# Optimization experiments

Measured on AMD Instinct MI355X. Metric: run time of the kernel, lower is better.

The kernel has to match this reference:

```python
import jax, jax.numpy as jnp
import numpy as np

B, S_ENC, S_DEC, D_ENC, D_DEC, UNITS = 8, 256, 128, 512, 512, 512


def setup_inputs() -> dict:
    key = jax.random.key(0)
    ks = jax.random.split(key, 5)
    enc_scale = 1.0 / np.sqrt(D_ENC)
    dec_scale = 1.0 / np.sqrt(D_DEC)
    u_scale = 1.0 / np.sqrt(UNITS)
    return {
        "encodings": jax.random.normal(ks[0], (B, S_ENC, D_ENC), dtype=jnp.float32),
        "decodings": jax.random.normal(ks[1], (B, S_DEC, D_DEC), dtype=jnp.float32),
        "W_enc": jax.random.normal(ks[2], (D_ENC, UNITS), dtype=jnp.float32) * enc_scale,
        "W_dec": jax.random.normal(ks[3], (D_DEC, UNITS), dtype=jnp.float32) * dec_scale,
        "W_score": jax.random.normal(ks[4], (UNITS, 1), dtype=jnp.float32) * u_scale,
        "bias_enc": jnp.zeros((UNITS,), dtype=jnp.float32),
        "bias_dec": jnp.zeros((UNITS,), dtype=jnp.float32),
        "bias_score": jnp.zeros((1,), dtype=jnp.float32),
    }


def reference(encodings, decodings, W_enc, W_dec, W_score, bias_enc, bias_dec, bias_score):
    # activation='linear' -> identity after the bias add
    d_enc = jnp.einsum("bed,du->beu", encodings, W_enc) + bias_enc  # [B, S_enc, U]
    d_dec = jnp.einsum("bqd,du->bqu", decodings, W_dec) + bias_dec  # [B, S_dec, U]
    # Bahdanau additive scores: tanh(dec_proj + enc_proj) broadcast to [B, S_dec, S_enc, U]
    tanh_add = jnp.tanh(d_dec[:, :, None, :] + d_enc[:, None, :, :])
    scores = jnp.einsum("bqeu,u->bqe", tanh_add, W_score[:, 0]) + bias_score[0]
    weights = jax.nn.softmax(scores, axis=-1)  # softmax over encoder positions
    # weighted sum of raw encodings -> [B, S_dec, D_enc]
    contexts = jnp.einsum("bqe,bed->bqd", weights, encodings)
    return contexts
```

## Files before the change

### kernel.cpp

```cpp
#include <hip/hip_runtime.h>
#include <hip/hip_fp16.h>

typedef __attribute__((ext_vector_type(8))) _Float16 f16x8;
typedef __attribute__((ext_vector_type(4))) float f32x4;
typedef __attribute__((ext_vector_type(2))) __fp16 fp16x2;

__device__ inline unsigned int pack_f16(float x, float y) {
    union { fp16x2 h; unsigned int u; } c;
    c.h = __builtin_amdgcn_cvt_pkrtz(x, y);
    return c.u;
}
__device__ inline float2 unpack_f16(unsigned int u) {
    union { unsigned int u32; __half2 h2; } c; c.u32 = u;
    return __half22float2(c.h2);
}

__global__ __launch_bounds__(256) void prep_w(
    const float* __restrict__ Wenc, const float* __restrict__ Wdec,
    const float* __restrict__ enc,  const float* __restrict__ dec,
    unsigned short* __restrict__ WeT, unsigned short* __restrict__ WdT,
    unsigned short* __restrict__ enc16, unsigned short* __restrict__ dec16)
{
    __shared__ float L[64][65];
    const int bid = blockIdx.x;
    const int t = threadIdx.x;
    if (bid >= 128) {
        const float* src; unsigned int* dst;
        if (bid < 192) { int blk = bid - 128; src = enc + (size_t)blk * 16384;
                         dst = (unsigned int*)enc16 + (size_t)blk * 8192; }
        else           { int blk = bid - 192; src = dec + (size_t)blk * 16384;
                         dst = (unsigned int*)dec16 + (size_t)blk * 8192; }
#pragma unroll 4
        for (int i = 0; i < 16; ++i) {
            int off = (i << 10) + (t << 2);
            float4 v = *(const float4*)(src + off);
            *(uint2*)(dst + (off >> 1)) =
                make_uint2(pack_f16(v.x, v.y), pack_f16(v.z, v.w));
        }
        return;
    }
    const float* W = (bid < 64) ? Wenc : Wdec;
    unsigned short* T = (bid < 64) ? WeT : WdT;
    const int tb = bid & 63;
    const int d0 = (tb >> 3) << 6, u0v = (tb & 7) << 6;
    {
        const int c4 = (t & 15) << 2;
#pragma unroll
        for (int i = 0; i < 4; ++i) {
            int row = (i << 4) + (t >> 4);
            float4 v = *(const float4*)&W[(size_t)(d0 + row) * 512 + u0v + c4];
            L[row][c4 + 0] = v.x;
            L[row][c4 + 1] = v.y;
            L[row][c4 + 2] = v.z;
            L[row][c4 + 3] = v.w;
        }
    }
    __syncthreads();
    const int u = t >> 2, dg = t & 3;
    unsigned int hw[8];
#pragma unroll
    for (int j = 0; j < 8; ++j) {
        float x0 = L[(dg << 4) + (j << 1) + 0][u];
        float x1 = L[(dg << 4) + (j << 1) + 1][u];
        hw[j] = pack_f16(x0, x1);
    }
    size_t ob = (size_t)(u0v + u) * 512 + d0 + (dg << 4);
    *(uint4*)&T[ob]     = make_uint4(hw[0], hw[1], hw[2], hw[3]);
    *(uint4*)&T[ob + 8] = make_uint4(hw[4], hw[5], hw[6], hw[7]);
}

__global__ __launch_bounds__(256, 3) void proj_kernel(
    const unsigned short* __restrict__ enc16, const unsigned short* __restrict__ dec16,
    const unsigned short* __restrict__ WeT,   const unsigned short* __restrict__ WdT,
    const float* __restrict__ bias_enc, const float* __restrict__ bias_dec,
    unsigned short* __restrict__ EH,
    float* __restrict__ Gq4)
{
    __shared__ float red[2][64][17];

    const float Cs = 2.8853900817779268f;
    const int bid = blockIdx.x;
    const int t = threadIdx.x;
    const int lane = t & 63, wv = t >> 6;
    const int th = wv & 1;
    const int kh = wv >> 1;
    const int koff = kh << 8;
    const int frow = lane & 15, quad = lane >> 4;
    const int ko = quad << 3;

    const unsigned short *pa0, *pa1, *pb0, *pb1;
    if (bid < 512) {
        const int b = bid & 7, s = bid >> 3;
        const int u0 = ((s & 7) << 6) + (th << 5);
        const int e0 = (s >> 3) << 5;
        pa0 = WeT + (size_t)(u0 + frow) * 512 + ko + koff;
        pa1 = pa0 + 16 * 512;
        pb0 = enc16 + (size_t)((b << 8) + e0 + frow) * 512 + ko + koff;
        pb1 = pb0 + 16 * 512;
    } else {
        const int s = bid - 512;
        const int b = s & 7, s2 = s >> 3;
        const int q0 = ((s2 >> 4) << 6) + (th << 5);
        const int u0 = (s2 & 15) << 5;
        pa0 = dec16 + (size_t)((b << 7) + q0 + frow) * 512 + ko + koff;
        pa1 = pa0 + 16 * 512;
        pb0 = WdT + (size_t)(u0 + frow) * 512 + ko + koff;
        pb1 = pb0 + 16 * 512;
    }

    f16x8 sa0[4], sa1[4], sb0[4], sb1[4];
    auto LD = [&](int st, int k) {
        sa0[st] = *(const f16x8*)(pa0 + k);
        sa1[st] = *(const f16x8*)(pa1 + k);
        sb0[st] = *(const f16x8*)(pb0 + k);
        sb1[st] = *(const f16x8*)(pb1 + k);
    };
    f32x4 acc[2][2] = {{{0.f,0.f,0.f,0.f},{0.f,0.f,0.f,0.f}},
                       {{0.f,0.f,0.f,0.f},{0.f,0.f,0.f,0.f}}};
    LD(0, 0); LD(1, 32); LD(2, 64); LD(3, 96);
    for (int k0 = 0; k0 < 256; k0 += 128) {
#pragma unroll
        for (int st = 0; st < 4; ++st) {
            acc[0][0] = __builtin_amdgcn_mfma_f32_16x16x32_f16(sa0[st], sb0[st], acc[0][0], 0, 0, 0);
            acc[0][1] = __builtin_amdgcn_mfma_f32_16x16x32_f16(sa0[st], sb1[st], acc[0][1], 0, 0, 0);
            acc[1][0] = __builtin_amdgcn_mfma_f32_16x16x32_f16(sa1[st], sb0[st], acc[1][0], 0, 0, 0);
            acc[1][1] = __builtin_amdgcn_mfma_f32_16x16x32_f16(sa1[st], sb1[st], acc[1][1], 0, 0, 0);
            LD(st, (k0 + 128 + (st << 5)) & 255);
        }
    }

    if (kh == 1) {
#pragma unroll
        for (int fm = 0; fm < 2; ++fm)
#pragma unroll
            for (int fn = 0; fn < 2; ++fn)
#pragma unroll
                for (int g = 0; g < 4; ++g)
                    red[th][lane][(((fm << 1) + fn) << 2) + g] = acc[fm][fn][g];
    }
    __syncthreads();
    if (kh == 1) return;
#pragma unroll
    for (int fm = 0; fm < 2; ++fm)
#pragma unroll
        for (int fn = 0; fn < 2; ++fn)
#pragma unroll
            for (int g = 0; g < 4; ++g)
                acc[fm][fn][g] += red[th][lane][(((fm << 1) + fn) << 2) + g];

    if (bid < 512) {
        const int b = bid & 7, s = bid >> 3;
        const int u0 = ((s & 7) << 6) + (th << 5);
        const int e0 = (s >> 3) << 5;
#pragma unroll
        for (int fm = 0; fm < 2; ++fm)
#pragma unroll
            for (int fn = 0; fn < 2; ++fn) {
                int ub = u0 + (fm << 4) + (quad << 2);
                int e  = e0 + (fn << 4) + frow;
                float4 bi = *(const float4*)&bias_enc[ub];
                float E0 = __builtin_amdgcn_exp2f((acc[fm][fn][0] + bi.x) * Cs);
                float E1 = __builtin_amdgcn_exp2f((acc[fm][fn][1] + bi.y) * Cs);
                float E2 = __builtin_amdgcn_exp2f((acc[fm][fn][2] + bi.z) * Cs);
                float E3 = __builtin_amdgcn_exp2f((acc[fm][fn][3] + bi.w) * Cs);
                ((uint2*)EH)[(((size_t)(b << 7) + (ub >> 2)) << 8) + e] =
                    make_uint2(pack_f16(E0, E1), pack_f16(E2, E3));
            }
    } else {
        const int s = bid - 512;
        const int b = s & 7, s2 = s >> 3;
        const int q0 = ((s2 >> 4) << 6) + (th << 5);
        const int u0 = (s2 & 15) << 5;
#pragma unroll
        for (int fm = 0; fm < 2; ++fm)
#pragma unroll
            for (int fn = 0; fn < 2; ++fn) {
                int qb = q0 + (fm << 4) + (quad << 2);
                int u  = u0 + (fn << 4) + frow;
                float bi = bias_dec[u];
                float G0 = __builtin_amdgcn_exp2f((acc[fm][fn][0] + bi) * Cs);
                float G1 = __builtin_amdgcn_exp2f((acc[fm][fn][1] + bi) * Cs);
                float G2 = __builtin_amdgcn_exp2f((acc[fm][fn][2] + bi) * Cs);
                float G3 = __builtin_amdgcn_exp2f((acc[fm][fn][3] + bi) * Cs);
                size_t base = (((size_t)(b << 5) + (qb >> 2)) << 11) + ((size_t)u << 2);
                *(float4*)&Gq4[base] = make_float4(G0, G1, G2, G3);
            }
    }
}

__global__ __launch_bounds__(1024, 4) void attend_kernel(
    const unsigned short* __restrict__ enc16,
    const unsigned short* __restrict__ EH,
    const float* __restrict__ Gq4,
    const float* __restrict__ Wscore,
    float* __restrict__ out)
{
    __shared__ float smem[8192];
    __shared__ float wT[256][4];

    const float LOG2E = 1.4426950408889634f;

    const int bid = blockIdx.x;
    const int b = bid & 7;
    const int qt = (bid >> 3) & 31;
    const int q0 = qt << 2;
    const int tid = threadIdx.x;
    const int wv = tid >> 6, lane = tid & 63;

    const int e  = ((wv & 3) << 6) + lane;
    const int uq = wv >> 2;
    const int u0 = __builtin_amdgcn_readfirstlane(uq << 7);

    const uint2* Ep = (const uint2*)EH + (((size_t)(b << 7) + (u0 >> 2)) << 8) + e;
    const float* Gq = Gq4 + (((size_t)(b << 5) + qt) << 11);
    const float* Wp = Wscore + u0;

    float a0 = 0.f, a1 = 0.f, a2 = 0.f, a3 = 0.f;
    uint2 deA = Ep[0];
    uint2 deB = Ep[1 << 8];
    float4 g0 = *(const float4*)(Gq + ((u0 + 0) << 2));
    float4 g1 = *(const float4*)(Gq + ((u0 + 1) << 2));
    float4 g2 = *(const float4*)(Gq + ((u0 + 2) << 2));
    float4 g3 = *(const float4*)(Gq + ((u0 + 3) << 2));
    float4 w4 = *(const float4*)(Wp);

    auto PROC = [&](uint2 cde, float4 cg0, float4 cg1, float4 cg2, float4 cg3,
                    float4 cw) {
        float2 f01 = unpack_f16(cde.x);
        float2 f23 = unpack_f16(cde.y);
        float E;
        E = f01.x;
        a0 = fmaf(cw.x, __builtin_amdgcn_rcpf(fmaf(E, cg0.x, 1.f)), a0);
        a1 = fmaf(cw.x, __builtin_amdgcn_rcpf(fmaf(E, cg0.y, 1.f)), a1);
        a2 = fmaf(cw.x, __builtin_amdgcn_rcpf(fmaf(E, cg0.z, 1.f)), a2);
        a3 = fmaf(cw.x, __builtin_amdgcn_rcpf(fmaf(E, cg0.w, 1.f)), a3);
        E = f01.y;
        a0 = fmaf(cw.y, __builtin_amdgcn_rcpf(fmaf(E, cg1.x, 1.f)), a0);
        a1 = fmaf(cw.y, __builtin_amdgcn_rcpf(fmaf(E, cg1.y, 1.f)), a1);
        a2 = fmaf(cw.y, __builtin_amdgcn_rcpf(fmaf(E, cg1.z, 1.f)), a2);
        a3 = fmaf(cw.y, __builtin_amdgcn_rcpf(fmaf(E, cg1.w, 1.f)), a3);
        E = f23.x;
        a0 = fmaf(cw.z, __builtin_amdgcn_rcpf(fmaf(E, cg2.x, 1.f)), a0);
        a1 = fmaf(cw.z, __builtin_amdgcn_rcpf(fmaf(E, cg2.y, 1.f)), a1);
        a2 = fmaf(cw.z, __builtin_amdgcn_rcpf(fmaf(E, cg2.z, 1.f)), a2);
        a3 = fmaf(cw.z, __builtin_amdgcn_rcpf(fmaf(E, cg2.w, 1.f)), a3);
        E = f23.y;
        a0 = fmaf(cw.w, __builtin_amdgcn_rcpf(fmaf(E, cg3.x, 1.f)), a0);
        a1 = fmaf(cw.w, __builtin_amdgcn_rcpf(fmaf(E, cg3.y, 1.f)), a1);
        a2 = fmaf(cw.w, __builtin_amdgcn_rcpf(fmaf(E, cg3.z, 1.f)), a2);
        a3 = fmaf(cw.w, __builtin_amdgcn_rcpf(fmaf(E, cg3.w, 1.f)), a3);
    };

    for (int g = 0; g < 32; g += 2) {
        uint2 cde = deA;
        float4 cg0 = g0, cg1 = g1, cg2 = g2, cg3 = g3, cw = w4;
        deA = Ep[(size_t)((g + 2) & 31) << 8];
        {
            int un = u0 + ((g + 1) << 2);
            g0 = *(const float4*)(Gq + ((un + 0) << 2));
            g1 = *(const float4*)(Gq + ((un + 1) << 2));
            g2 = *(const float4*)(Gq + ((un + 2) << 2));
            g3 = *(const float4*)(Gq + ((un + 3) << 2));
            w4 = *(const float4*)(Wp + ((g + 1) << 2));
        }
        PROC(cde, cg0, cg1, cg2, cg3, cw);

        cde = deB;
        cg0 = g0; cg1 = g1; cg2 = g2; cg3 = g3; cw = w4;
        deB = Ep[(size_t)((g + 3) & 31) << 8];
        if (g < 30) {
            int un = u0 + ((g + 2) << 2);
            g0 = *(const float4*)(Gq + ((un + 0) << 2));
            g1 = *(const float4*)(Gq + ((un + 1) << 2));
            g2 = *(const float4*)(Gq + ((un + 2) << 2));
            g3 = *(const float4*)(Gq + ((un + 3) << 2));
            w4 = *(const float4*)(Wp + ((g + 2) << 2));
        }
        PROC(cde, cg0, cg1, cg2, cg3, cw);
    }
    smem[((uq << 2) + 0) * 256 + e] = a0;
    smem[((uq << 2) + 1) * 256 + e] = a1;
    smem[((uq << 2) + 2) * 256 + e] = a2;
    smem[((uq << 2) + 3) * 256 + e] = a3;
    __syncthreads();

    if (wv < 4) {
        const int q = wv;
        float l[4];
        float m = -1e30f;
#pragma unroll
        for (int i = 0; i < 4; ++i) {
            int ee = lane + (i << 6);
            float a = smem[(0 + q) * 256 + ee] + smem[(4 + q) * 256 + ee] +
                      smem[(8 + q) * 256 + ee] + smem[(12 + q) * 256 + ee];
            l[i] = -2.f * a;
            m = fmaxf(m, l[i]);
        }
#pragma unroll
        for (int mk = 32; mk >= 1; mk >>= 1) m = fmaxf(m, __shfl_xor(m, mk, 64));
        float p[4];
        float ssum = 0.f;
#pragma unroll
        for (int i = 0; i < 4; ++i) {
            p[i] = __builtin_amdgcn_exp2f((l[i] - m) * LOG2E);
            ssum += p[i];
        }
#pragma unroll
        for (int mk = 32; mk >= 1; mk >>= 1) ssum += __shfl_xor(ssum, mk, 64);
        float inv = __builtin_amdgcn_rcpf(ssum);
#pragma unroll
        for (int i = 0; i < 4; ++i) wT[lane + (i << 6)][q] = p[i] * inv;
    }
    __syncthreads();

    {
        const int dp = tid & 255;
        float p0x = 0.f, p0y = 0.f, p1x = 0.f, p1y = 0.f;
        float p2x = 0.f, p2y = 0.f, p3x = 0.f, p3y = 0.f;
        const unsigned int* ep = (const unsigned int*)enc16 +
                                 (((size_t)(b << 8) + (uq << 6)) << 8) + dp;
#pragma unroll 4
        for (int ee = 0; ee < 64; ++ee) {
            float2 x = unpack_f16(ep[(size_t)ee << 8]);
            float4 w = *(const float4*)&wT[(uq << 6) + ee][0];
            p0x = fmaf(w.x, x.x, p0x); p0y = fmaf(w.x, x.y, p0y);
            p1x = fmaf(w.y, x.x, p1x); p1y = fmaf(w.y, x.y, p1y);
            p2x = fmaf(w.z, x.x, p2x); p2y = fmaf(w.z, x.y, p2y);
            p3x = fmaf(w.w, x.x, p3x); p3y = fmaf(w.w, x.y, p3y);
        }
        float2* sc = (float2*)smem;
        sc[((uq << 2) + 0) * 256 + dp] = make_float2(p0x, p0y);
        sc[((uq << 2) + 1) * 256 + dp] = make_float2(p1x, p1y);
        sc[((uq << 2) + 2) * 256 + dp] = make_float2(p2x, p2y);
        sc[((uq << 2) + 3) * 256 + dp] = make_float2(p3x, p3y);
        __syncthreads();
        const int q = tid >> 8;
        float2 s0 = sc[(0 + q) * 256 + dp];
        float2 s1 = sc[(4 + q) * 256 + dp];
        float2 s2 = sc[(8 + q) * 256 + dp];
        float2 s3 = sc[(12 + q) * 256 + dp];
        float2 o = make_float2(s0.x + s1.x + s2.x + s3.x,
                               s0.y + s1.y + s2.y + s3.y);
        *(float2*)&out[(size_t)((b << 7) + q0 + q) * 512 + (dp << 1)] = o;
    }
}

extern "C" void kernel_launch(void* const* d_in, const int* in_sizes, int n_in,
                              void* d_out, int out_size, void* d_ws, size_t ws_size,
                              hipStream_t stream) {
    const float* enc      = (const float*)d_in[0];
    const float* dec      = (const float*)d_in[1];
    const float* Wenc     = (const float*)d_in[2];
    const float* Wdec     = (const float*)d_in[3];
    const float* Wscore   = (const float*)d_in[4];
    const float* bias_enc = (const float*)d_in[5];
    const float* bias_dec = (const float*)d_in[6];
    float* out = (float*)d_out;

    float* ws = (float*)d_ws;
    unsigned short* EH  = (unsigned short*)ws;
    float* Gq4          = ws + 524288;
    unsigned short* WeT = (unsigned short*)(ws + 1048576);
    unsigned short* WdT = WeT + 262144;
    unsigned short* enc16 = WdT + 262144;
    unsigned short* dec16 = enc16 + 1048576;

    prep_w<<<224, 256, 0, stream>>>(Wenc, Wdec, enc, dec, WeT, WdT, enc16, dec16);
    proj_kernel<<<768, 256, 0, stream>>>(enc16, dec16, WeT, WdT,
                                         bias_enc, bias_dec, EH, Gq4);
    attend_kernel<<<256, 1024, 0, stream>>>(enc16, EH, Gq4, Wscore, out);
}
```

Before: 111.7 us.

## Replace split-K projection with 64x64 output tiles per block

Each projection block now computes a 64x64 output tile, with four waves arranged 2x2 and each wave running the full K=512 loop. Previously two wave pairs each covered half of K and combined partial sums through shared memory. The change removes the LDS reduction and the barrier, and halves the block count from 768 to 384. In exchange each wave runs a K loop twice as long, there are fewer blocks to spread across CUs, and the occupancy hint drops to 2.

```diff
diff --git a/kernel.cpp b/kernel.cpp
--- a/kernel.cpp
+++ b/kernel.cpp
@@ -69,42 +69,38 @@
     *(uint4*)&T[ob + 8] = make_uint4(hw[4], hw[5], hw[6], hw[7]);
 }
 
-__global__ __launch_bounds__(256, 3) void proj_kernel(
+__global__ __launch_bounds__(256, 2) void proj_kernel(
     const unsigned short* __restrict__ enc16, const unsigned short* __restrict__ dec16,
     const unsigned short* __restrict__ WeT,   const unsigned short* __restrict__ WdT,
     const float* __restrict__ bias_enc, const float* __restrict__ bias_dec,
     unsigned short* __restrict__ EH,
     float* __restrict__ Gq4)
 {
-    __shared__ float red[2][64][17];
-
     const float Cs = 2.8853900817779268f;
     const int bid = blockIdx.x;
     const int t = threadIdx.x;
     const int lane = t & 63, wv = t >> 6;
-    const int th = wv & 1;
-    const int kh = wv >> 1;
-    const int koff = kh << 8;
+    const int wy = wv >> 1, wx = wv & 1;
     const int frow = lane & 15, quad = lane >> 4;
     const int ko = quad << 3;
 
     const unsigned short *pa0, *pa1, *pb0, *pb1;
-    if (bid < 512) {
+    if (bid < 256) {
         const int b = bid & 7, s = bid >> 3;
-        const int u0 = ((s & 7) << 6) + (th << 5);
-        const int e0 = (s >> 3) << 5;
-        pa0 = WeT + (size_t)(u0 + frow) * 512 + ko + koff;
+        const int u0 = (s >> 2) << 6;
+        const int e0 = (s & 3) << 6;
+        pa0 = WeT + (size_t)(u0 + (wy << 5) + frow) * 512 + ko;
         pa1 = pa0 + 16 * 512;
-        pb0 = enc16 + (size_t)((b << 8) + e0 + frow) * 512 + ko + koff;
+        pb0 = enc16 + (size_t)((b << 8) + e0 + (wx << 5) + frow) * 512 + ko;
         pb1 = pb0 + 16 * 512;
     } else {
-        const int s = bid - 512;
+        const int s = bid - 256;
         const int b = s & 7, s2 = s >> 3;
-        const int q0 = ((s2 >> 4) << 6) + (th << 5);
-        const int u0 = (s2 & 15) << 5;
-        pa0 = dec16 + (size_t)((b << 7) + q0 + frow) * 512 + ko + koff;
+        const int q0 = (s2 >> 3) << 6;
+        const int u0 = (s2 & 7) << 6;
+        pa0 = dec16 + (size_t)((b << 7) + q0 + (wy << 5) + frow) * 512 + ko;
         pa1 = pa0 + 16 * 512;
-        pb0 = WdT + (size_t)(u0 + frow) * 512 + ko + koff;
+        pb0 = WdT + (size_t)(u0 + (wx << 5) + frow) * 512 + ko;
         pb1 = pb0 + 16 * 512;
     }
 
@@ -118,46 +114,26 @@
     f32x4 acc[2][2] = {{{0.f,0.f,0.f,0.f},{0.f,0.f,0.f,0.f}},
                        {{0.f,0.f,0.f,0.f},{0.f,0.f,0.f,0.f}}};
     LD(0, 0); LD(1, 32); LD(2, 64); LD(3, 96);
-    for (int k0 = 0; k0 < 256; k0 += 128) {
+    for (int k0 = 0; k0 < 512; k0 += 128) {
 #pragma unroll
         for (int st = 0; st < 4; ++st) {
             acc[0][0] = __builtin_amdgcn_mfma_f32_16x16x32_f16(sa0[st], sb0[st], acc[0][0], 0, 0, 0);
             acc[0][1] = __builtin_amdgcn_mfma_f32_16x16x32_f16(sa0[st], sb1[st], acc[0][1], 0, 0, 0);
             acc[1][0] = __builtin_amdgcn_mfma_f32_16x16x32_f16(sa1[st], sb0[st], acc[1][0], 0, 0, 0);
             acc[1][1] = __builtin_amdgcn_mfma_f32_16x16x32_f16(sa1[st], sb1[st], acc[1][1], 0, 0, 0);
-            LD(st, (k0 + 128 + (st << 5)) & 255);
-        }
-    }
-
-    if (kh == 1) {
+            LD(st, (k0 + 128 + (st << 5)) & 511);
+        }
+    }
+
+    if (bid < 256) {
+        const int b = bid & 7, s = bid >> 3;
+        const int u0 = (s >> 2) << 6, e0 = (s & 3) << 6;
 #pragma unroll
         for (int fm = 0; fm < 2; ++fm)
 #pragma unroll
-            for (int fn = 0; fn < 2; ++fn)
-#pragma unroll
-                for (int g = 0; g < 4; ++g)
-                    red[th][lane][(((fm << 1) + fn) << 2) + g] = acc[fm][fn][g];
-    }
-    __syncthreads();
-    if (kh == 1) return;
-#pragma unroll
-    for (int fm = 0; fm < 2; ++fm)
-#pragma unroll
-        for (int fn = 0; fn < 2; ++fn)
-#pragma unroll
-            for (int g = 0; g < 4; ++g)
-                acc[fm][fn][g] += red[th][lane][(((fm << 1) + fn) << 2) + g];
-
-    if (bid < 512) {
-        const int b = bid & 7, s = bid >> 3;
-        const int u0 = ((s & 7) << 6) + (th << 5);
-        const int e0 = (s >> 3) << 5;
-#pragma unroll
-        for (int fm = 0; fm < 2; ++fm)
-#pragma unroll
             for (int fn = 0; fn < 2; ++fn) {
-                int ub = u0 + (fm << 4) + (quad << 2);
-                int e  = e0 + (fn << 4) + frow;
+                int ub = u0 + (wy << 5) + (fm << 4) + (quad << 2);
+                int e  = e0 + (wx << 5) + (fn << 4) + frow;
                 float4 bi = *(const float4*)&bias_enc[ub];
                 float E0 = __builtin_amdgcn_exp2f((acc[fm][fn][0] + bi.x) * Cs);
                 float E1 = __builtin_amdgcn_exp2f((acc[fm][fn][1] + bi.y) * Cs);
@@ -167,16 +143,15 @@
                     make_uint2(pack_f16(E0, E1), pack_f16(E2, E3));
             }
     } else {
-        const int s = bid - 512;
+        const int s = bid - 256;
         const int b = s & 7, s2 = s >> 3;
-        const int q0 = ((s2 >> 4) << 6) + (th << 5);
-        const int u0 = (s2 & 15) << 5;
+        const int q0 = (s2 >> 3) << 6, u0 = (s2 & 7) << 6;
 #pragma unroll
         for (int fm = 0; fm < 2; ++fm)
 #pragma unroll
             for (int fn = 0; fn < 2; ++fn) {
-                int qb = q0 + (fm << 4) + (quad << 2);
-                int u  = u0 + (fn << 4) + frow;
+                int qb = q0 + (wy << 5) + (fm << 4) + (quad << 2);
+                int u  = u0 + (wx << 5) + (fn << 4) + frow;
                 float bi = bias_dec[u];
                 float G0 = __builtin_amdgcn_exp2f((acc[fm][fn][0] + bi) * Cs);
                 float G1 = __builtin_amdgcn_exp2f((acc[fm][fn][1] + bi) * Cs);
@@ -366,7 +341,7 @@
     unsigned short* dec16 = enc16 + 1048576;
 
     prep_w<<<224, 256, 0, stream>>>(Wenc, Wdec, enc, dec, WeT, WdT, enc16, dec16);
-    proj_kernel<<<768, 256, 0, stream>>>(enc16, dec16, WeT, WdT,
+    proj_kernel<<<384, 256, 0, stream>>>(enc16, dec16, WeT, WdT,
                                          bias_enc, bias_dec, EH, Gq4);
     attend_kernel<<<256, 1024, 0, stream>>>(enc16, EH, Gq4, Wscore, out);
 }
```

Result: slower. 114.7 us (+2.8%).
